# Performance work log

Measured on AMD Instinct MI355X. Metric: run time of the kernel, lower is better.

## Reference

```python
import jax, jax.numpy as jnp
import numpy as np

NEG_INF = -1e9
LRELU_SLOPE = 0.2  # torch GAT default leaky_relu negative slope


def setup_inputs() -> dict:
    key = jax.random.key(0)
    k1, k2, k3, k4, k5 = jax.random.split(key, 5)
    N, F_IN, H, DH = 4096, 1433, 8, 8  # n_nodes, in_features, n_heads, per-head dim (n_hidden=64)
    vert = jax.random.normal(k1, (N, F_IN), dtype=jnp.float32)
    edge = jax.random.randint(k2, (N, N), 0, 2, dtype=jnp.int32)  # dense adjacency mask
    W = jax.random.normal(k3, (F_IN, H * DH), dtype=jnp.float32) * 0.05
    a_l = jax.random.normal(k4, (H, DH), dtype=jnp.float32) * 0.05
    a_r = jax.random.normal(k5, (H, DH), dtype=jnp.float32) * 0.05
    return {"vert": vert, "edge": edge, "W": W, "a_l": a_l, "a_r": a_r}


def reference(vert, edge, W, a_l, a_r):
    # GAT-style edge-affinity layer (is_concat=True) + ELU; dropout is identity (eval mode).
    N = vert.shape[0]
    H, DH = a_l.shape
    g = (vert @ W).reshape(N, H, DH)                      # [N,H,Dh] projected node features
    sl = jnp.einsum('nhd,hd->nh', g, a_l)                 # source-node attention term
    sr = jnp.einsum('nhd,hd->nh', g, a_r)                 # target-node attention term
    e = sl[:, None, :] + sr[None, :, :]                   # [N,N,H]: attn([g_i || g_j])
    e = jnp.where(e >= 0, e, LRELU_SLOPE * e)             # leaky_relu
    mask = (edge != 0)[:, :, None]                        # [N,N,1]
    e = jnp.where(mask, e, NEG_INF)                       # mask non-edges
    a = jax.nn.softmax(e, axis=1)                         # normalize over neighbors j
    out = jnp.einsum('ijh,jhd->ihd', a, g).reshape(N, H * DH)  # aggregate + concat heads
    return jax.nn.elu(out)
```

## Files before the change

### kernel.cpp

```cpp
#include <hip/hip_runtime.h>
#include <hip/hip_bf16.h>

#define NN 4096
#define FIN 1433
#define NH 8
#define DH 8
#define HD 64
#define KP 1472
#define LOG2E 1.44269504f
#define NJS 8
#define ITB 32
#define NCHK ((NN / NJS) / 64)
#define NKS 4

typedef unsigned int u32;
typedef unsigned long long u64;
typedef float v4f __attribute__((ext_vector_type(4)));
typedef _Float16 f16;
typedef _Float16 h2 __attribute__((ext_vector_type(2)));
typedef _Float16 f16x8 __attribute__((ext_vector_type(8)));

static __device__ __forceinline__ short f2h16(float f) {
    union { f16 h; short s; } u; u.h = (f16)f; return u.s;
}
static __device__ __forceinline__ h2 u2h2(u32 x) {
    union { u32 u; h2 h; } v; v.u = x; return v.h;
}
static __device__ __forceinline__ u32 h22u(h2 x) {
    union { h2 h; u32 u; } v; v.h = x; return v.u;
}

#if __has_builtin(__builtin_amdgcn_sbfe)
#define SBFE1(x, k) __builtin_amdgcn_sbfe((int)(x), (k), 1)
#else
#define SBFE1(x, k) (((int)((x) << (31 - (k)))) >> 31)
#endif

static __device__ __forceinline__ void gload_lds16(const void* g, void* l) {
    __builtin_amdgcn_global_load_lds(
        (const __attribute__((address_space(1))) void*)g,
        (__attribute__((address_space(3))) void*)l, 16, 0, 0);
}

__global__ __launch_bounds__(256) void k_wprep(const float* __restrict__ W,
                                               short* __restrict__ Wt) {
    __shared__ float Ts[64][65];
    const int c = blockIdx.x;
    const int u = threadIdx.x;
    const int n4 = (u & 15) * 4;
    const int kr = u >> 4;
#pragma unroll
    for (int q = 0; q < 4; ++q) {
        const int kl = kr + q * 16;
        const int kg = c * 64 + kl;
        v4f v = {0.f, 0.f, 0.f, 0.f};
        if (kg < FIN) v = *(const v4f*)&W[(size_t)kg * HD + n4];
        *(v4f*)&Ts[kl][n4] = v;
    }
    __syncthreads();
    const int n = u >> 2;
    const int koff = (u & 3) * 16;
    __align__(16) short tmp[16];
#pragma unroll
    for (int r = 0; r < 16; ++r) tmp[r] = f2h16(Ts[koff + r][n]);
    *(uint4*)&Wt[(size_t)n * KP + c * 64 + koff]     = *(uint4*)&tmp[0];
    *(uint4*)&Wt[(size_t)n * KP + c * 64 + koff + 8] = *(uint4*)&tmp[8];
}

__global__ __launch_bounds__(256, 4) void k_gemm(
    const float* __restrict__ vert, const short* __restrict__ Wt,
    float* __restrict__ Cp)
{
    __shared__ float cacc[4][16][68];

    const int t = threadIdx.x, lane = t & 63, w = t >> 6;
    const int ml = lane & 15, q = lane >> 4;
    const int i0 = blockIdx.x * 16;
    const int ks = blockIdx.y;
    const float* vrow = vert + (size_t)(i0 + ml) * FIN;

    v4f acc[4];
#pragma unroll
    for (int g = 0; g < 4; ++g) acc[g] = (v4f){0.f, 0.f, 0.f, 0.f};

    for (int c = ks + 4 * w; c < 45; c += 16) {
        const int k0 = c * 32 + q * 8;
        v4f a0, a1;
        if (k0 + 7 < FIN) {
            a0 = *(const v4f*)&vrow[k0];
            a1 = *(const v4f*)&vrow[k0 + 4];
        } else {
            float tmp[8];
#pragma unroll
            for (int e = 0; e < 8; ++e)
                tmp[e] = (k0 + e < FIN) ? vrow[k0 + e] : 0.f;
            a0 = (v4f){tmp[0], tmp[1], tmp[2], tmp[3]};
            a1 = (v4f){tmp[4], tmp[5], tmp[6], tmp[7]};
        }
        const f16x8 af = {(f16)a0.x, (f16)a0.y, (f16)a0.z, (f16)a0.w,
                          (f16)a1.x, (f16)a1.y, (f16)a1.z, (f16)a1.w};
#pragma unroll
        for (int g = 0; g < 4; ++g) {
            const f16x8 bf = *(const f16x8*)&Wt[(size_t)(g * 16 + ml) * KP + k0];
            acc[g] = __builtin_amdgcn_mfma_f32_16x16x32_f16(af, bf, acc[g], 0, 0, 0);
        }
    }

#pragma unroll
    for (int g = 0; g < 4; ++g)
#pragma unroll
        for (int r = 0; r < 4; ++r)
            cacc[w][q * 4 + r][g * 16 + ml] = acc[g][r];
    __syncthreads();

    const int m = t >> 4, n4 = (t & 15) * 4;
    v4f s = (v4f){0.f, 0.f, 0.f, 0.f};
#pragma unroll
    for (int ww = 0; ww < 4; ++ww) s += *(const v4f*)&cacc[ww][m][n4];
    *(v4f*)&Cp[((size_t)ks * NN + i0 + m) * HD + n4] = s;
}

__global__ __launch_bounds__(256) void k_gpost(
    const float* __restrict__ Cp,
    const float* __restrict__ al, const float* __restrict__ ar,
    short* __restrict__ gT, short* __restrict__ eB, short* __restrict__ eD,
    float* __restrict__ Rw)
{
    const int t = threadIdx.x;
    const int gid = blockIdx.x * 256 + t;
    const int i = gid >> 4, n4 = (gid & 15) * 4;

    v4f s = (v4f){0.f, 0.f, 0.f, 0.f};
#pragma unroll
    for (int ks = 0; ks < NKS; ++ks)
        s += *(const v4f*)&Cp[((size_t)ks * NN + i) * HD + n4];

#pragma unroll
    for (int e = 0; e < 4; ++e)
        gT[(size_t)(n4 + e) * NN + i] = f2h16(s[e]);

    float pl = s.x * al[n4] + s.y * al[n4 + 1] + s.z * al[n4 + 2] + s.w * al[n4 + 3];
    float pr = s.x * ar[n4] + s.y * ar[n4 + 1] + s.z * ar[n4 + 2] + s.w * ar[n4 + 3];
    pl += __shfl_xor(pl, 1, 64);
    pr += __shfl_xor(pr, 1, 64);
    if ((t & 1) == 0) {
        const int h = (t & 15) >> 1;
        eB[h * NN + i] = f2h16(exp2f(pr * LOG2E));
        eD[h * NN + i] = f2h16(exp2f(0.2f * pr * LOG2E));
        Rw[i * NH + h] = exp2f(-0.8f * pl * LOG2E);
    }
}

__global__ __launch_bounds__(256, 4) void k_attn(
    const int* __restrict__ edge, const short* __restrict__ gT,
    const short* __restrict__ eB, const short* __restrict__ eD,
    const float* __restrict__ Rw,
    float* __restrict__ numw, float* __restrict__ denw)
{
    __shared__ __align__(16) short Gs[2][64 * 64];
    __shared__ __align__(16) short BDs[2][8 * 128];
    __shared__ __align__(16) u64 Ms[2][ITB];

    const int t = threadIdx.x, lane = t & 63, w = t >> 6;
    const int ml = lane & 15, quad = lane >> 4;
    const int m8 = ml & 7;
    const int i0 = blockIdx.x * ITB;
    const int js = blockIdx.y;
    const int jbase = js * (NN / NJS);
    const int h0 = w, h1 = w + 4;
    const bool mhi = (ml >= 8);
    const u32 one2 = 0x3C003C00u;
    const uint4 ones4 = (uint4){one2, one2, one2, one2};

    h2 Ri[2][2];
#pragma unroll
    for (int sub = 0; sub < 2; ++sub) {
        const f16 r0 = (f16)Rw[(i0 + sub * 16 + ml) * NH + h0];
        const f16 r1 = (f16)Rw[(i0 + sub * 16 + ml) * NH + h1];
        Ri[sub][0] = (h2){r0, r0};
        Ri[sub][1] = (h2){r1, r1};
    }

    const short *gsrc0, *gsrc1;
    {
        int u = t, row = u >> 3;
        gsrc0 = gT + (size_t)row * NN + jbase + (((u & 7) * 8) ^ ((row & 7) * 8));
        u = 256 + t; row = u >> 3;
        gsrc1 = gT + (size_t)row * NN + jbase + (((u & 7) * 8) ^ ((row & 7) * 8));
    }
    const short* bdsrc = nullptr;
    if (t < 128) {
        const int head = t >> 4, slot = t & 15;
        bdsrc = (slot < 8 ? eB : eD) + (size_t)head * NN + jbase + (slot & 7) * 8;
    }
    const int wub = (t & ~63) * 16;

    const int* ebase = edge + (size_t)(i0 + w * 8) * NN + jbase + lane;
    u32 er[8];

#define STAGE(buf, ck)                                                        \
    do {                                                                      \
        const int jc_ = (ck) * 64;                                            \
        gload_lds16(gsrc0 + jc_, (char*)Gs[buf] + wub);                       \
        gload_lds16(gsrc1 + jc_, (char*)Gs[buf] + 4096 + wub);                \
        if (t < 128) gload_lds16(bdsrc + jc_, (char*)BDs[buf] + wub);         \
    } while (0)

#define ELOAD(ck)                                                             \
    do {                                                                      \
        const int jo_ = (ck) * 64;                                            \
        _Pragma("unroll")                                                     \
        for (int rr = 0; rr < 8; ++rr)                                        \
            er[rr] = __builtin_nontemporal_load(ebase + (size_t)rr * NN + jo_); \
    } while (0)

#define EBALLOT(buf)                                                          \
    do {                                                                      \
        _Pragma("unroll")                                                     \
        for (int rr = 0; rr < 8; ++rr) {                                      \
            const u64 b_ = __ballot(er[rr] != 0);                             \
            if (lane == 0) Ms[buf][w * 8 + rr] = b_;                          \
        }                                                                     \
    } while (0)

    v4f acc[2][2];
#pragma unroll
    for (int sub = 0; sub < 2; ++sub) {
        acc[sub][0] = (v4f){0.f, 0.f, 0.f, 0.f};
        acc[sub][1] = (v4f){0.f, 0.f, 0.f, 0.f};
    }

    STAGE(0, 0);
    ELOAD(0);
    EBALLOT(0);

    for (int c = 0; c < NCHK; ++c) {
        const int cb = c & 1, nb = cb ^ 1;
        __syncthreads();
        const bool pf = (c + 1) < NCHK;
        if (pf) { STAGE(nb, c + 1); ELOAD(c + 1); }

        union { u64 q; uint2 d; } m0u, m1u;
        m0u.q = Ms[cb][ml];
        m1u.q = Ms[cb][16 + ml];

#pragma unroll
        for (int s = 0; s < 2; ++s) {
            const int xj = s * 32 + quad * 8;
            const int xg = xj ^ (m8 * 8);
            union { uint4 u; f16x8 h; } g0u, g1u;
            g0u.u = mhi ? ones4 : *(const uint4*)&Gs[cb][(h0 * 8 + m8) * 64 + xg];
            g1u.u = mhi ? ones4 : *(const uint4*)&Gs[cb][(h1 * 8 + m8) * 64 + xg];
            const uint4 bu0 = *(const uint4*)&BDs[cb][h0 * 128 + xj];
            const uint4 du0 = *(const uint4*)&BDs[cb][h0 * 128 + 64 + xj];
            const uint4 bu1 = *(const uint4*)&BDs[cb][h1 * 128 + xj];
            const uint4 du1 = *(const uint4*)&BDs[cb][h1 * 128 + 64 + xj];
#pragma unroll
            for (int sub = 0; sub < 2; ++sub) {
                const u32 half = sub ? ((s ? m1u.d.y : m1u.d.x))
                                     : ((s ? m0u.d.y : m0u.d.x));
                const u32 w8 = half >> (quad * 8);
                u32 m[4];
#pragma unroll
                for (int k = 0; k < 4; ++k) {
                    const int ea = SBFE1(w8, 2 * k);
                    const int eb = SBFE1(w8, 2 * k + 1);
                    m[k] = __builtin_amdgcn_perm((u32)eb, (u32)ea, 0x05040100u);
                }
                u32 aw0[4], aw1[4];
#pragma unroll
                for (int k = 0; k < 4; ++k) {
                    const u32 rd0 = h22u(Ri[sub][0] * u2h2((&du0.x)[k]));
                    const u32 rd1 = h22u(Ri[sub][1] * u2h2((&du1.x)[k]));
                    u32 p0, p1;
                    asm("v_pk_max_f16 %0, %1, %2" : "=v"(p0) : "v"(rd0), "v"((&bu0.x)[k]));
                    asm("v_pk_max_f16 %0, %1, %2" : "=v"(p1) : "v"(rd1), "v"((&bu1.x)[k]));
                    aw0[k] = p0 & m[k];
                    aw1[k] = p1 & m[k];
                }
                union { uint4 u; f16x8 h; } a0u, a1u;
                a0u.u = (uint4){aw0[0], aw0[1], aw0[2], aw0[3]};
                a1u.u = (uint4){aw1[0], aw1[1], aw1[2], aw1[3]};
                acc[sub][0] = __builtin_amdgcn_mfma_f32_16x16x32_f16(
                    a0u.h, g0u.h, acc[sub][0], 0, 0, 0);
                acc[sub][1] = __builtin_amdgcn_mfma_f32_16x16x32_f16(
                    a1u.h, g1u.h, acc[sub][1], 0, 0, 0);
            }
        }
        if (pf) EBALLOT(nb);
    }
#undef STAGE
#undef ELOAD
#undef EBALLOT

    float* nw = numw + (size_t)js * NN * HD;
    float* dw = denw + (size_t)js * NN * NH;
#pragma unroll
    for (int sub = 0; sub < 2; ++sub) {
        const int ibase = i0 + sub * 16 + quad * 4;
#pragma unroll
        for (int hh = 0; hh < 2; ++hh) {
            const int h = w + hh * 4;
#pragma unroll
            for (int r = 0; r < 4; ++r) {
                if (ml < 8)       nw[(ibase + r) * HD + h * 8 + ml] = acc[sub][hh][r];
                else if (ml == 8) dw[(ibase + r) * NH + h]          = acc[sub][hh][r];
            }
        }
    }
}

__global__ __launch_bounds__(256) void k_comb(
    const float* __restrict__ numw, const float* __restrict__ denw,
    float* __restrict__ out)
{
    const int gid = blockIdx.x * 256 + threadIdx.x;
    const int i = gid >> 6, h = (gid & 63) >> 3;
    float num = 0.f, den = 0.f;
#pragma unroll
    for (int s = 0; s < NJS; ++s) {
        num += numw[(size_t)s * NN * HD + gid];
        den += denw[(size_t)s * NN * NH + i * NH + h];
    }
    float x = num / den;
    out[gid] = (x > 0.f) ? x : (__expf(x) - 1.f);
}

extern "C" void kernel_launch(void* const* d_in, const int* in_sizes, int n_in,
                              void* d_out, int out_size, void* d_ws, size_t ws_size,
                              hipStream_t stream) {
    const float* vert = (const float*)d_in[0];
    const int*   edge = (const int*)d_in[1];
    const float* W    = (const float*)d_in[2];
    const float* al   = (const float*)d_in[3];
    const float* ar   = (const float*)d_in[4];
    float* out = (float*)d_out;

    char* ws = (char*)d_ws;
    short* gT    = (short*)ws;
    short* eB    = (short*)(ws + 512 * 1024);
    short* eD    = (short*)(ws + 576 * 1024);
    float* Rw    = (float*)(ws + 640 * 1024);
    short* Wt    = (short*)(ws + 768 * 1024);
    float* Cp    = (float*)(ws + 3 * 1024 * 1024);
    float* numw  = (float*)(ws + 7 * 1024 * 1024);
    float* denw  = (float*)(ws + 15 * 1024 * 1024);

    hipLaunchKernelGGL(k_wprep, dim3(23), dim3(256), 0, stream, W, Wt);
    hipLaunchKernelGGL(k_gemm, dim3(NN / 16, NKS), dim3(256), 0, stream,
                       vert, Wt, Cp);
    hipLaunchKernelGGL(k_gpost, dim3(NN * 16 / 256), dim3(256), 0, stream,
                       Cp, al, ar, gT, eB, eD, Rw);
    hipLaunchKernelGGL(k_attn, dim3(NN / ITB, NJS), dim3(256), 0, stream,
                       edge, gT, eB, eD, Rw, numw, denw);
    hipLaunchKernelGGL(k_comb, dim3(NN * HD / 256), dim3(256), 0, stream,
                       numw, denw, out);
}
```

Measured before the change: 150.1 us.

## Halve attention row tile, single-buffer LDS, prefetch edge mask two chunks ahead

```diff
diff --git a/kernel.cpp b/kernel.cpp
--- a/kernel.cpp
+++ b/kernel.cpp
@@ -9,7 +9,7 @@
 #define KP 1472
 #define LOG2E 1.44269504f
 #define NJS 8
-#define ITB 32
+#define ITB 16
 #define NCHK ((NN / NJS) / 64)
 #define NKS 4
 
@@ -151,15 +151,15 @@
     }
 }
 
-__global__ __launch_bounds__(256, 4) void k_attn(
+__global__ __launch_bounds__(256, 8) void k_attn(
     const int* __restrict__ edge, const short* __restrict__ gT,
     const short* __restrict__ eB, const short* __restrict__ eD,
     const float* __restrict__ Rw,
     float* __restrict__ numw, float* __restrict__ denw)
 {
-    __shared__ __align__(16) short Gs[2][64 * 64];
-    __shared__ __align__(16) short BDs[2][8 * 128];
-    __shared__ __align__(16) u64 Ms[2][ITB];
+    __shared__ __align__(16) short Gs[64 * 64];
+    __shared__ __align__(16) short BDs[8 * 128];
+    __shared__ __align__(16) u64 Ms[ITB];
 
     const int t = threadIdx.x, lane = t & 63, w = t >> 6;
     const int ml = lane & 15, quad = lane >> 4;
@@ -172,13 +172,12 @@
     const u32 one2 = 0x3C003C00u;
     const uint4 ones4 = (uint4){one2, one2, one2, one2};
 
-    h2 Ri[2][2];
-#pragma unroll
-    for (int sub = 0; sub < 2; ++sub) {
-        const f16 r0 = (f16)Rw[(i0 + sub * 16 + ml) * NH + h0];
-        const f16 r1 = (f16)Rw[(i0 + sub * 16 + ml) * NH + h1];
-        Ri[sub][0] = (h2){r0, r0};
-        Ri[sub][1] = (h2){r1, r1};
+    h2 Ri[2];
+    {
+        const f16 r0 = (f16)Rw[(i0 + ml) * NH + h0];
+        const f16 r1 = (f16)Rw[(i0 + ml) * NH + h1];
+        Ri[0] = (h2){r0, r0};
+        Ri[1] = (h2){r1, r1};
     }
 
     const short *gsrc0, *gsrc1;
@@ -195,99 +194,101 @@
     }
     const int wub = (t & ~63) * 16;
 
-    const int* ebase = edge + (size_t)(i0 + w * 8) * NN + jbase + lane;
-    u32 er[8];
-
-#define STAGE(buf, ck)                                                        \
+    const int* ebase = edge + (size_t)(i0 + w * 4) * NN + jbase + lane;
+    u32 er[4];
+
+#define STAGE(ck)                                                             \
     do {                                                                      \
         const int jc_ = (ck) * 64;                                            \
-        gload_lds16(gsrc0 + jc_, (char*)Gs[buf] + wub);                       \
-        gload_lds16(gsrc1 + jc_, (char*)Gs[buf] + 4096 + wub);                \
-        if (t < 128) gload_lds16(bdsrc + jc_, (char*)BDs[buf] + wub);         \
+        gload_lds16(gsrc0 + jc_, (char*)Gs + wub);                            \
+        gload_lds16(gsrc1 + jc_, (char*)Gs + 4096 + wub);                     \
+        if (t < 128) gload_lds16(bdsrc + jc_, (char*)BDs + wub);              \
     } while (0)
 
 #define ELOAD(ck)                                                             \
     do {                                                                      \
         const int jo_ = (ck) * 64;                                            \
         _Pragma("unroll")                                                     \
-        for (int rr = 0; rr < 8; ++rr)                                        \
+        for (int rr = 0; rr < 4; ++rr)                                        \
             er[rr] = __builtin_nontemporal_load(ebase + (size_t)rr * NN + jo_); \
     } while (0)
 
-#define EBALLOT(buf)                                                          \
+#define EBALLOT()                                                             \
     do {                                                                      \
         _Pragma("unroll")                                                     \
-        for (int rr = 0; rr < 8; ++rr) {                                      \
+        for (int rr = 0; rr < 4; ++rr) {                                      \
             const u64 b_ = __ballot(er[rr] != 0);                             \
-            if (lane == 0) Ms[buf][w * 8 + rr] = b_;                          \
+            if (lane == 0) Ms[w * 4 + rr] = b_;                               \
         }                                                                     \
     } while (0)
 
-    v4f acc[2][2];
-#pragma unroll
-    for (int sub = 0; sub < 2; ++sub) {
-        acc[sub][0] = (v4f){0.f, 0.f, 0.f, 0.f};
-        acc[sub][1] = (v4f){0.f, 0.f, 0.f, 0.f};
-    }
-
-    STAGE(0, 0);
+    v4f acc[2];
+    acc[0] = (v4f){0.f, 0.f, 0.f, 0.f};
+    acc[1] = (v4f){0.f, 0.f, 0.f, 0.f};
+
     ELOAD(0);
-    EBALLOT(0);
+    EBALLOT();
+    STAGE(0);
+    ELOAD(1);
+    asm volatile("s_waitcnt vmcnt(4) lgkmcnt(0)" ::: "memory");
+    __builtin_amdgcn_sched_barrier(0);
+    __builtin_amdgcn_s_barrier();
+    __builtin_amdgcn_sched_barrier(0);
 
     for (int c = 0; c < NCHK; ++c) {
-        const int cb = c & 1, nb = cb ^ 1;
-        __syncthreads();
-        const bool pf = (c + 1) < NCHK;
-        if (pf) { STAGE(nb, c + 1); ELOAD(c + 1); }
-
-        union { u64 q; uint2 d; } m0u, m1u;
-        m0u.q = Ms[cb][ml];
-        m1u.q = Ms[cb][16 + ml];
-
+        const u64 mask64 = Ms[ml];
 #pragma unroll
         for (int s = 0; s < 2; ++s) {
             const int xj = s * 32 + quad * 8;
             const int xg = xj ^ (m8 * 8);
             union { uint4 u; f16x8 h; } g0u, g1u;
-            g0u.u = mhi ? ones4 : *(const uint4*)&Gs[cb][(h0 * 8 + m8) * 64 + xg];
-            g1u.u = mhi ? ones4 : *(const uint4*)&Gs[cb][(h1 * 8 + m8) * 64 + xg];
-            const uint4 bu0 = *(const uint4*)&BDs[cb][h0 * 128 + xj];
-            const uint4 du0 = *(const uint4*)&BDs[cb][h0 * 128 + 64 + xj];
-            const uint4 bu1 = *(const uint4*)&BDs[cb][h1 * 128 + xj];
-            const uint4 du1 = *(const uint4*)&BDs[cb][h1 * 128 + 64 + xj];
-#pragma unroll
-            for (int sub = 0; sub < 2; ++sub) {
-                const u32 half = sub ? ((s ? m1u.d.y : m1u.d.x))
-                                     : ((s ? m0u.d.y : m0u.d.x));
-                const u32 w8 = half >> (quad * 8);
-                u32 m[4];
-#pragma unroll
-                for (int k = 0; k < 4; ++k) {
-                    const int ea = SBFE1(w8, 2 * k);
-                    const int eb = SBFE1(w8, 2 * k + 1);
-                    m[k] = __builtin_amdgcn_perm((u32)eb, (u32)ea, 0x05040100u);
-                }
-                u32 aw0[4], aw1[4];
-#pragma unroll
-                for (int k = 0; k < 4; ++k) {
-                    const u32 rd0 = h22u(Ri[sub][0] * u2h2((&du0.x)[k]));
-                    const u32 rd1 = h22u(Ri[sub][1] * u2h2((&du1.x)[k]));
-                    u32 p0, p1;
-                    asm("v_pk_max_f16 %0, %1, %2" : "=v"(p0) : "v"(rd0), "v"((&bu0.x)[k]));
-                    asm("v_pk_max_f16 %0, %1, %2" : "=v"(p1) : "v"(rd1), "v"((&bu1.x)[k]));
-                    aw0[k] = p0 & m[k];
-                    aw1[k] = p1 & m[k];
-                }
-                union { uint4 u; f16x8 h; } a0u, a1u;
-                a0u.u = (uint4){aw0[0], aw0[1], aw0[2], aw0[3]};
-                a1u.u = (uint4){aw1[0], aw1[1], aw1[2], aw1[3]};
-                acc[sub][0] = __builtin_amdgcn_mfma_f32_16x16x32_f16(
-                    a0u.h, g0u.h, acc[sub][0], 0, 0, 0);
-                acc[sub][1] = __builtin_amdgcn_mfma_f32_16x16x32_f16(
-                    a1u.h, g1u.h, acc[sub][1], 0, 0, 0);
+            g0u.u = mhi ? ones4 : *(const uint4*)&Gs[(h0 * 8 + m8) * 64 + xg];
+            g1u.u = mhi ? ones4 : *(const uint4*)&Gs[(h1 * 8 + m8) * 64 + xg];
+            const uint4 bu0 = *(const uint4*)&BDs[h0 * 128 + xj];
+            const uint4 du0 = *(const uint4*)&BDs[h0 * 128 + 64 + xj];
+            const uint4 bu1 = *(const uint4*)&BDs[h1 * 128 + xj];
+            const uint4 du1 = *(const uint4*)&BDs[h1 * 128 + 64 + xj];
+            const u32 w8 = (u32)(mask64 >> (s * 32 + quad * 8));
+            u32 m[4];
+#pragma unroll
+            for (int k = 0; k < 4; ++k) {
+                const int ea = SBFE1(w8, 2 * k);
+                const int eb = SBFE1(w8, 2 * k + 1);
+                m[k] = __builtin_amdgcn_perm((u32)eb, (u32)ea, 0x05040100u);
             }
-        }
-        if (pf) EBALLOT(nb);
+            u32 aw0[4], aw1[4];
+#pragma unroll
+            for (int k = 0; k < 4; ++k) {
+                const u32 rd0 = h22u(Ri[0] * u2h2((&du0.x)[k]));
+                const u32 rd1 = h22u(Ri[1] * u2h2((&du1.x)[k]));
+                u32 p0, p1;
+                asm("v_pk_max_f16 %0, %1, %2" : "=v"(p0) : "v"(rd0), "v"((&bu0.x)[k]));
+                asm("v_pk_max_f16 %0, %1, %2" : "=v"(p1) : "v"(rd1), "v"((&bu1.x)[k]));
+                aw0[k] = p0 & m[k];
+                aw1[k] = p1 & m[k];
+            }
+            union { uint4 u; f16x8 h; } a0u, a1u;
+            a0u.u = (uint4){aw0[0], aw0[1], aw0[2], aw0[3]};
+            a1u.u = (uint4){aw1[0], aw1[1], aw1[2], aw1[3]};
+            acc[0] = __builtin_amdgcn_mfma_f32_16x16x32_f16(a0u.h, g0u.h, acc[0], 0, 0, 0);
+            acc[1] = __builtin_amdgcn_mfma_f32_16x16x32_f16(a1u.h, g1u.h, acc[1], 0, 0, 0);
+        }
+        if (c + 1 == NCHK) break;
+
+        __builtin_amdgcn_sched_barrier(0);
+        __builtin_amdgcn_s_barrier();
+        __builtin_amdgcn_sched_barrier(0);
+        EBALLOT();
+        STAGE(c + 1);
+        if (c + 2 < NCHK) {
+            ELOAD(c + 2);
+            asm volatile("s_waitcnt vmcnt(4) lgkmcnt(0)" ::: "memory");
+        } else {
+            asm volatile("s_waitcnt vmcnt(0) lgkmcnt(0)" ::: "memory");
+        }
+        __builtin_amdgcn_sched_barrier(0);
+        __builtin_amdgcn_s_barrier();
+        __builtin_amdgcn_sched_barrier(0);
     }
 #undef STAGE
 #undef ELOAD
@@ -295,17 +296,14 @@
 
     float* nw = numw + (size_t)js * NN * HD;
     float* dw = denw + (size_t)js * NN * NH;
-#pragma unroll
-    for (int sub = 0; sub < 2; ++sub) {
-        const int ibase = i0 + sub * 16 + quad * 4;
-#pragma unroll
-        for (int hh = 0; hh < 2; ++hh) {
-            const int h = w + hh * 4;
-#pragma unroll
-            for (int r = 0; r < 4; ++r) {
-                if (ml < 8)       nw[(ibase + r) * HD + h * 8 + ml] = acc[sub][hh][r];
-                else if (ml == 8) dw[(ibase + r) * NH + h]          = acc[sub][hh][r];
-            }
+    const int ibase = i0 + quad * 4;
+#pragma unroll
+    for (int hh = 0; hh < 2; ++hh) {
+        const int h = w + hh * 4;
+#pragma unroll
+        for (int r = 0; r < 4; ++r) {
+            if (ml < 8)       nw[(ibase + r) * HD + h * 8 + ml] = acc[hh][r];
+            else if (ml == 8) dw[(ibase + r) * NH + h]          = acc[hh][r];
         }
     }
 }
```

Result: slower. 153.2 us (+2.1%).
